# Optimization experiments

Hardware: AMD Instinct MI355X
Metric: run time of the kernel (lower is better)

The kernel has to match this reference:

```python
import jax, jax.numpy as jnp
import numpy as np

ALPHA = 1.0
BETA = 1.0
GAMMA = 1.0
EPS = 1e-08

D = 128      # feature / hash-code dim
N = 4096     # number of items


def setup_inputs() -> dict:
    key = jax.random.key(0)
    k = jax.random.split(key, 6)
    return {
        "SU": jax.random.uniform(k[0], (N, N, 1), dtype=jnp.float32),
        "SP": jax.random.uniform(k[1], (N, N, 1), dtype=jnp.float32),
        "SM": jax.random.uniform(k[2], (N, N, 1), dtype=jnp.float32),
        "FP": jax.random.uniform(k[3], (D, N), dtype=jnp.float32),
        "FM": jax.random.uniform(k[4], (D, N), dtype=jnp.float32),
        "B": jax.random.uniform(k[5], (D, N), dtype=jnp.float32),
    }


def reference(SU, SP, SM, FP, FM, B):
    # IRSC: Omega_U = FP^T FM / 2, sum over all (i,j) of -S*Omega + log(1+Omega)
    omega_u = jnp.einsum('di,dj->ij', FP, FM) * 0.5          # [N, N]
    loss_irsc = jnp.sum(-SU[:, :, 0] * omega_u + jnp.log1p(omega_u))

    # IASC: same form on FP^T FP and FM^T FM, with epsilon inside the log
    omega_p = jnp.einsum('di,dj->ij', FP, FP) * 0.5
    omega_m = jnp.einsum('di,dj->ij', FM, FM) * 0.5
    loss_sp = jnp.sum(-SP[:, :, 0] * omega_p + jnp.log(1.0 + omega_p + EPS))
    loss_sm = jnp.sum(-SM[:, :, 0] * omega_m + jnp.log(1.0 + omega_m + EPS))
    loss_iasc = loss_sp + loss_sm

    # BQC: Frobenius norms (not squared)
    loss_bqc = jnp.sqrt(jnp.sum((FP - B) ** 2)) + jnp.sqrt(jnp.sum((FM - B) ** 2))

    # FDC: ||F @ ones||_F^2 = sum over rows of (row-sum)^2
    loss_fdc = jnp.sum(jnp.sum(FP, axis=1) ** 2) + jnp.sum(jnp.sum(FM, axis=1) ** 2)

    return loss_irsc + ALPHA * loss_iasc + BETA * loss_bqc + GAMMA * loss_fdc
```

## Files before the change

kernel.cpp:

```cpp
#include <hip/hip_runtime.h>
#include <hip/hip_bf16.h>
#include <math.h>

#define NN 4096
#define DD 128

typedef __attribute__((ext_vector_type(8))) short bf16x8;
typedef __attribute__((ext_vector_type(4))) float f32x4;

__device__ __forceinline__ void gload_lds16(const float* g, float* l) {
    __builtin_amdgcn_global_load_lds((const __attribute__((address_space(1))) char*)g,
                                     (__attribute__((address_space(3))) char*)l, 16, 0, 0);
}

__global__ __launch_bounds__(256)
void convert_kernel(const float* __restrict__ FP, const float* __restrict__ FM,
                    __hip_bfloat16* __restrict__ FPb, __hip_bfloat16* __restrict__ FMb)
{
    const float* src = blockIdx.y ? FM : FP;
    __hip_bfloat16* dst = blockIdx.y ? FMb : FPb;
    const int t  = threadIdx.x;
    const int il = t & 127;
    const int dh = t >> 7;
    const int i  = blockIdx.x * 128 + il;
    #pragma unroll
    for (int it = 0; it < 8; ++it) {
        const int d0 = dh * 64 + it * 8;
        union { __hip_bfloat162 h[4]; bf16x8 v; } p;
        #pragma unroll
        for (int j = 0; j < 4; ++j) {
            const float a = src[(long)(d0 + 2*j)     * NN + i];
            const float b = src[(long)(d0 + 2*j + 1) * NN + i];
            p.h[j] = __float22bfloat162_rn(make_float2(a, b));
        }
        *(bf16x8*)&dst[(long)i * DD + d0] = p.v;
    }
}

__global__ __launch_bounds__(256, 2)
void gemm_loss_mfma2(const float* __restrict__ SU, const float* __restrict__ SP,
                     const float* __restrict__ SM,
                     const __hip_bfloat16* __restrict__ FPb,
                     const __hip_bfloat16* __restrict__ FMb,
                     double* __restrict__ accum)
{
    __shared__ float sS[4][64 * 64];
    __shared__ float red[4];
    const int t    = threadIdx.x;
    const int lane = t & 63, wid = t >> 6;
    const int wr   = wid >> 1, wc = wid & 1;
    const int l15  = lane & 15, l4 = lane >> 4;
    const int z    = blockIdx.z;
    const float* S  = (z == 0) ? SU : (z == 1) ? SP : SM;
    const short* Fa = (const short*)((z == 2) ? FMb : FPb);
    const short* Fb = (const short*)((z == 0) ? FMb : (z == 1) ? FPb : (const __hip_bfloat16*)FMb);
    const float eps = (z == 0) ? 0.0f : 1e-8f;
    const int i0 = blockIdx.y * 128;
    const int j0 = blockIdx.x * 128;

    bf16x8 af[4][4], bg[4][4];
    {
        const long ibase = (long)(i0 + wr * 64 + l15) * DD;
        const long jbase = (long)(j0 + wc * 64 + l15) * DD;
        #pragma unroll
        for (int kb = 0; kb < 4; ++kb) {
            const int ko = kb * 32 + l4 * 8;
            #pragma unroll
            for (int m = 0; m < 4; ++m) {
                af[kb][m] = *(const bf16x8*)&Fa[ibase + (long)m * 16 * DD + ko];
                bg[kb][m] = *(const bf16x8*)&Fb[jbase + (long)m * 16 * DD + ko];
            }
        }
    }

    {
        float* qb = sS[wid];
        const float* gb = S + (long)(i0 + wr * 64 + l4) * NN + j0 + wc * 64 + l15 * 4;
        #pragma unroll
        for (int q = 0; q < 16; ++q)
            gload_lds16(gb + (long)q * 4 * NN, qb + q * 256);
    }
    __builtin_amdgcn_sched_barrier(0);

    f32x4 acc[4][4] = {};
    #pragma unroll
    for (int kb = 0; kb < 4; ++kb)
        #pragma unroll
        for (int m = 0; m < 4; ++m)
            #pragma unroll
            for (int n = 0; n < 4; ++n)
                acc[m][n] = __builtin_amdgcn_mfma_f32_16x16x32_bf16(af[kb][m], bg[kb][n], acc[m][n], 0, 0, 0);

    asm volatile("s_waitcnt vmcnt(0)" ::: "memory");
    __builtin_amdgcn_sched_barrier(0);

    float lsum = 0.f;
    const float* q = sS[wid];
    #pragma unroll
    for (int m = 0; m < 4; ++m)
        #pragma unroll
        for (int n = 0; n < 4; ++n) {
            const int base = (m * 16 + l4 * 4) * 64 + n * 16 + l15;
            #pragma unroll
            for (int r = 0; r < 4; ++r) {
                const float s = q[base + r * 64];
                const float o = 0.5f * acc[m][n][r];
                lsum += fmaf(-s, o, __logf(1.0f + o + eps));
            }
        }

    float v = lsum;
    #pragma unroll
    for (int off = 32; off; off >>= 1) v += __shfl_down(v, off);
    if ((t & 63) == 0) red[t >> 6] = v;
    __syncthreads();
    if (t == 0) {
        const float tot = red[0] + red[1] + red[2] + red[3];
        atomicAdd(accum, (double)tot);
    }
}

__global__ __launch_bounds__(256, 2)
void gemm_loss_mfma(const float* __restrict__ S, const float* __restrict__ F1,
                    const float* __restrict__ F2, float eps, double* __restrict__ accum)
{
    __shared__ char lds[2][128 * 256];
    __shared__ float red[4];
    const int t  = threadIdx.x;
    const int i0 = blockIdx.y * 128;
    const int j0 = blockIdx.x * 128;
    {
        const int il   = t & 127;
        const int half = t >> 7;
        const float* c1 = F1 + i0 + il;
        const float* c2 = F2 + j0 + il;
        char* r1 = lds[0] + il * 256;
        char* r2 = lds[1] + il * 256;
        #pragma unroll
        for (int it = 0; it < 8; ++it) {
            const int q  = half * 8 + it;
            const int d0 = q * 8;
            float a[8], b[8];
            #pragma unroll
            for (int j = 0; j < 8; ++j) {
                a[j] = c1[(long)(d0 + j) * NN];
                b[j] = c2[(long)(d0 + j) * NN];
            }
            union { __hip_bfloat162 h[4]; bf16x8 v; } pa, pb;
            #pragma unroll
            for (int j = 0; j < 4; ++j) {
                pa.h[j] = __float22bfloat162_rn(make_float2(a[2*j], a[2*j+1]));
                pb.h[j] = __float22bfloat162_rn(make_float2(b[2*j], b[2*j+1]));
            }
            const int off = (q ^ (il & 15)) << 4;
            *(bf16x8*)(r1 + off) = pa.v;
            *(bf16x8*)(r2 + off) = pb.v;
        }
    }
    __syncthreads();
    const int lane = t & 63;
    const int wid  = t >> 6;
    const int wr   = wid >> 1, wc = wid & 1;
    const int l15  = lane & 15, l4 = lane >> 4;
    float sreg[4][4][4];
    #pragma unroll
    for (int am = 0; am < 4; ++am)
        #pragma unroll
        for (int r = 0; r < 4; ++r) {
            const long gi   = (long)(i0 + wr * 64 + am * 16 + l4 * 4 + r);
            const long base = gi * NN + j0 + wc * 64 + l15;
            #pragma unroll
            for (int bn = 0; bn < 4; ++bn)
                sreg[am][bn][r] = S[base + bn * 16];
        }
    f32x4 acc[4][4] = {};
    #pragma unroll
    for (int kb = 0; kb < 4; ++kb) {
        bf16x8 af[4], bgr[4];
        #pragma unroll
        for (int m = 0; m < 4; ++m) {
            const int ia = wr * 64 + m * 16 + l15;
            af[m] = *(const bf16x8*)(lds[0] + ia * 256 + (((kb * 4 + l4) ^ l15) << 4));
            const int jb = wc * 64 + m * 16 + l15;
            bgr[m] = *(const bf16x8*)(lds[1] + jb * 256 + (((kb * 4 + l4) ^ l15) << 4));
        }
        #pragma unroll
        for (int m = 0; m < 4; ++m)
            #pragma unroll
            for (int n = 0; n < 4; ++n)
                acc[m][n] = __builtin_amdgcn_mfma_f32_16x16x32_bf16(af[m], bgr[n], acc[m][n], 0, 0, 0);
    }
    float lsum = 0.f;
    #pragma unroll
    for (int m = 0; m < 4; ++m)
        #pragma unroll
        for (int n = 0; n < 4; ++n)
            #pragma unroll
            for (int r = 0; r < 4; ++r) {
                const float o = 0.5f * acc[m][n][r];
                lsum += fmaf(-sreg[m][n][r], o, __logf(1.0f + o + eps));
            }
    float v = lsum;
    #pragma unroll
    for (int off = 32; off; off >>= 1) v += __shfl_down(v, off);
    if ((t & 63) == 0) red[t >> 6] = v;
    __syncthreads();
    if (t == 0) {
        const float tot = red[0] + red[1] + red[2] + red[3];
        atomicAdd(accum, (double)tot);
    }
}

__global__ __launch_bounds__(256)
void bqc_kernel(const float* __restrict__ FP, const float* __restrict__ FM,
                const float* __restrict__ B, double* __restrict__ ws)
{
    __shared__ float red1[4], red2[4];
    const int n4 = DD * NN / 4;
    float s1 = 0.f, s2 = 0.f;
    for (int i = blockIdx.x * blockDim.x + threadIdx.x; i < n4;
         i += gridDim.x * blockDim.x) {
        const float4 p = ((const float4*)FP)[i];
        const float4 m = ((const float4*)FM)[i];
        const float4 b = ((const float4*)B)[i];
        float d;
        d = p.x - b.x; s1 += d * d;  d = p.y - b.y; s1 += d * d;
        d = p.z - b.z; s1 += d * d;  d = p.w - b.w; s1 += d * d;
        d = m.x - b.x; s2 += d * d;  d = m.y - b.y; s2 += d * d;
        d = m.z - b.z; s2 += d * d;  d = m.w - b.w; s2 += d * d;
    }
    const int t = threadIdx.x;
    #pragma unroll
    for (int off = 32; off; off >>= 1) {
        s1 += __shfl_down(s1, off);
        s2 += __shfl_down(s2, off);
    }
    if ((t & 63) == 0) { red1[t >> 6] = s1; red2[t >> 6] = s2; }
    __syncthreads();
    if (t == 0) {
        atomicAdd(&ws[1], (double)(red1[0] + red1[1] + red1[2] + red1[3]));
        atomicAdd(&ws[2], (double)(red2[0] + red2[1] + red2[2] + red2[3]));
    }
}

__global__ __launch_bounds__(256)
void fdc_kernel(const float* __restrict__ FP, const float* __restrict__ FM,
                double* __restrict__ ws)
{
    __shared__ float red[4];
    const float* F = (blockIdx.x >= DD) ? FM : FP;
    const int row = blockIdx.x & (DD - 1);
    float s = 0.f;
    const float4* rowp = (const float4*)&F[(long)row * NN];
    for (int i = threadIdx.x; i < NN / 4; i += blockDim.x) {
        const float4 v = rowp[i];
        s += v.x + v.y + v.z + v.w;
    }
    const int t = threadIdx.x;
    #pragma unroll
    for (int off = 32; off; off >>= 1) s += __shfl_down(s, off);
    if ((t & 63) == 0) red[t >> 6] = s;
    __syncthreads();
    if (t == 0) {
        const double rs = (double)(red[0] + red[1] + red[2] + red[3]);
        atomicAdd(&ws[3], rs * rs);
    }
}

__global__ void finalize_kernel(const double* __restrict__ ws, float* __restrict__ out)
{
    if (threadIdx.x == 0 && blockIdx.x == 0)
        out[0] = (float)(ws[0] + ws[3] + sqrt(ws[1]) + sqrt(ws[2]));
}

extern "C" void kernel_launch(void* const* d_in, const int* in_sizes, int n_in,
                              void* d_out, int out_size, void* d_ws, size_t ws_size,
                              hipStream_t stream)
{
    const float* SU = (const float*)d_in[0];
    const float* SP = (const float*)d_in[1];
    const float* SM = (const float*)d_in[2];
    const float* FP = (const float*)d_in[3];
    const float* FM = (const float*)d_in[4];
    const float* B  = (const float*)d_in[5];
    float*  out = (float*)d_out;
    double* ws  = (double*)d_ws;

    hipMemsetAsync(d_ws, 0, 4 * sizeof(double), stream);

    const size_t fb_bytes = (size_t)NN * DD * sizeof(__hip_bfloat16);
    const size_t need     = 4096 + 2 * fb_bytes;

    if (ws_size >= need) {
        __hip_bfloat16* FPb = (__hip_bfloat16*)((char*)d_ws + 4096);
        __hip_bfloat16* FMb = (__hip_bfloat16*)((char*)d_ws + 4096 + fb_bytes);
        convert_kernel<<<dim3(NN / 128, 2), 256, 0, stream>>>(FP, FM, FPb, FMb);
        gemm_loss_mfma2<<<dim3(NN / 128, NN / 128, 3), 256, 0, stream>>>(
            SU, SP, SM, FPb, FMb, ws);
    } else {
        dim3 grid(NN / 128, NN / 128);
        gemm_loss_mfma<<<grid, 256, 0, stream>>>(SU, FP, FM, 0.0f, ws);
        gemm_loss_mfma<<<grid, 256, 0, stream>>>(SP, FP, FP, 1e-8f, ws);
        gemm_loss_mfma<<<grid, 256, 0, stream>>>(SM, FM, FM, 1e-8f, ws);
    }
    bqc_kernel<<<512, 256, 0, stream>>>(FP, FM, B, ws);
    fdc_kernel<<<256, 256, 0, stream>>>(FP, FM, ws);
    finalize_kernel<<<1, 64, 0, stream>>>(ws, out);
}
```

Measured before the change: 98.69 us.

## Split loss into symmetric log-term GEMM and reassociated S·F dot-product pass

Splits the fused GEMM+loss into two kernels. The log1p term is computed over upper-triangular tiles only for the symmetric FP^T FP and FM^T FM cases, with off-diagonal tiles weighted by two. The -S*Omega term is reassociated as sum(F_a ⊙ (S · F_b^T)) and computed by a skinny MFMA kernel that streams S once, converted to bf16 on the fly. Atomics are spread over 16 padded slots to cut contention. This removes about a third of the log GEMM work, but S is now rounded to bf16, which adds precision error, and an extra conversion kernel is added.

```diff
diff --git a/kernel.cpp b/kernel.cpp
--- a/kernel.cpp
+++ b/kernel.cpp
@@ -8,17 +8,13 @@
 typedef __attribute__((ext_vector_type(8))) short bf16x8;
 typedef __attribute__((ext_vector_type(4))) float f32x4;
 
-__device__ __forceinline__ void gload_lds16(const float* g, float* l) {
-    __builtin_amdgcn_global_load_lds((const __attribute__((address_space(1))) char*)g,
-                                     (__attribute__((address_space(3))) char*)l, 16, 0, 0);
-}
 
 __global__ __launch_bounds__(256)
-void convert_kernel(const float* __restrict__ FP, const float* __restrict__ FM,
-                    __hip_bfloat16* __restrict__ FPb, __hip_bfloat16* __restrict__ FMb)
+void convert_t_kernel(const float* __restrict__ FP, const float* __restrict__ FM,
+                      __hip_bfloat16* __restrict__ FPt, __hip_bfloat16* __restrict__ FMt)
 {
     const float* src = blockIdx.y ? FM : FP;
-    __hip_bfloat16* dst = blockIdx.y ? FMb : FPb;
+    __hip_bfloat16* dst = blockIdx.y ? FMt : FPt;
     const int t  = threadIdx.x;
     const int il = t & 127;
     const int dh = t >> 7;
@@ -37,87 +33,197 @@
     }
 }
 
-__global__ __launch_bounds__(256, 2)
-void gemm_loss_mfma2(const float* __restrict__ SU, const float* __restrict__ SP,
-                     const float* __restrict__ SM,
-                     const __hip_bfloat16* __restrict__ FPb,
-                     const __hip_bfloat16* __restrict__ FMb,
-                     double* __restrict__ accum)
-{
-    __shared__ float sS[4][64 * 64];
-    __shared__ float red[4];
-    const int t    = threadIdx.x;
+__global__ __launch_bounds__(256)
+void convert_d_kernel(const float* __restrict__ FP, const float* __restrict__ FM,
+                      __hip_bfloat16* __restrict__ FPd, __hip_bfloat16* __restrict__ FMd)
+{
+    const int total = DD * NN / 4;
+    for (int idx = blockIdx.x * blockDim.x + threadIdx.x; idx < 2 * total;
+         idx += gridDim.x * blockDim.x) {
+        const bool second = idx >= total;
+        const float4 v = ((const float4*)(second ? FM : FP))[second ? idx - total : idx];
+        union { __hip_bfloat162 h[2]; uint2 u; } p;
+        p.h[0] = __float22bfloat162_rn(make_float2(v.x, v.y));
+        p.h[1] = __float22bfloat162_rn(make_float2(v.z, v.w));
+        ((uint2*)(second ? FMd : FPd))[second ? idx - total : idx] = p.u;
+    }
+}
+
+__global__ __launch_bounds__(256, 3)
+void log_kernel(const __hip_bfloat16* __restrict__ FPt_,
+                const __hip_bfloat16* __restrict__ FMt_, double* __restrict__ accum)
+{
+    const int bid = blockIdx.x;
+    int z, ti, tj;
+    if (bid < 1024) { z = 0; ti = bid >> 5; tj = bid & 31; }
+    else {
+        int q = bid - 1024;
+        z = 1 + (q >= 528);
+        int u = (q >= 528) ? q - 528 : q;
+        ti = 0;
+        while (u >= 32 - ti) { u -= 32 - ti; ++ti; }
+        tj = ti + u;
+    }
+    const short* Fa = (const short*)((z == 2) ? FMt_ : FPt_);
+    const short* Fb = (const short*)((z == 0) ? FMt_ : (z == 1) ? FPt_ : FMt_);
+    const float onep = 1.0f + ((z == 0) ? 0.0f : 1e-8f);
+
+    const int t = threadIdx.x;
     const int lane = t & 63, wid = t >> 6;
-    const int wr   = wid >> 1, wc = wid & 1;
-    const int l15  = lane & 15, l4 = lane >> 4;
-    const int z    = blockIdx.z;
+    const int wr = wid >> 1, wc = wid & 1;
+    const int l15 = lane & 15, l4 = lane >> 4;
+    const int i0 = ti * 128 + wr * 64;
+    const int j0 = tj * 128 + wc * 64;
+
+    const bool diagTile = (z > 0) && (ti == tj);
+    const bool skip     = diagTile && (wr > wc);
+    const bool perElem  = diagTile && (wr == wc);
+    const bool dbl      = (z > 0) && ((ti < tj) || (diagTile && wr < wc));
+
+    const short* pa = Fa + (long)(i0 + l15) * DD + l4 * 8;
+    const short* pb = Fb + (long)(j0 + l15) * DD + l4 * 8;
+
+    float lsum = 0.f;
+    if (!skip) {
+        bf16x8 Aa[4], Ab[4], Ba[4], Bb[4];
+        #pragma unroll
+        for (int m = 0; m < 4; ++m) {
+            Aa[m] = *(const bf16x8*)(pa + m * (16 * DD));
+            Ab[m] = *(const bf16x8*)(pb + m * (16 * DD));
+        }
+        f32x4 acc[4][4] = {};
+        #pragma unroll
+        for (int kb = 0; kb < 4; ++kb) {
+            if (kb == 0 || kb == 2) {
+                if (kb < 3) {
+                    #pragma unroll
+                    for (int m = 0; m < 4; ++m) {
+                        Ba[m] = *(const bf16x8*)(pa + m * (16 * DD) + (kb + 1) * 32);
+                        Bb[m] = *(const bf16x8*)(pb + m * (16 * DD) + (kb + 1) * 32);
+                    }
+                }
+                #pragma unroll
+                for (int m = 0; m < 4; ++m)
+                    #pragma unroll
+                    for (int n = 0; n < 4; ++n)
+                        acc[m][n] = __builtin_amdgcn_mfma_f32_16x16x32_bf16(Aa[m], Ab[n], acc[m][n], 0, 0, 0);
+            } else {
+                if (kb < 3) {
+                    #pragma unroll
+                    for (int m = 0; m < 4; ++m) {
+                        Aa[m] = *(const bf16x8*)(pa + m * (16 * DD) + (kb + 1) * 32);
+                        Ab[m] = *(const bf16x8*)(pb + m * (16 * DD) + (kb + 1) * 32);
+                    }
+                }
+                #pragma unroll
+                for (int m = 0; m < 4; ++m)
+                    #pragma unroll
+                    for (int n = 0; n < 4; ++n)
+                        acc[m][n] = __builtin_amdgcn_mfma_f32_16x16x32_bf16(Ba[m], Bb[n], acc[m][n], 0, 0, 0);
+            }
+        }
+        #pragma unroll
+        for (int m = 0; m < 4; ++m)
+            #pragma unroll
+            for (int n = 0; n < 4; ++n)
+                #pragma unroll
+                for (int r = 0; r < 4; ++r) {
+                    const float term = __logf(fmaf(0.5f, acc[m][n][r], onep));
+                    if (perElem) {
+                        const int il = m * 16 + l4 * 4 + r;
+                        const int jl = n * 16 + l15;
+                        const float w = (jl > il) ? 2.f : ((jl == il) ? 1.f : 0.f);
+                        lsum = fmaf(w, term, lsum);
+                    } else {
+                        lsum += term;
+                    }
+                }
+        if (dbl) lsum *= 2.f;
+    }
+
+    float v = lsum;
+    #pragma unroll
+    for (int off = 32; off; off >>= 1) v += __shfl_down(v, off);
+    if (lane == 0 && !skip)
+        atomicAdd(accum + ((bid & 15) << 3), (double)v);
+}
+
+__global__ __launch_bounds__(256, 3)
+void dot_kernel(const float* __restrict__ SU, const float* __restrict__ SP,
+                const float* __restrict__ SM,
+                const __hip_bfloat16* __restrict__ FPd_,
+                const __hip_bfloat16* __restrict__ FMd_,
+                const float* __restrict__ FPf, const float* __restrict__ FMf,
+                double* __restrict__ accum)
+{
+    const int t = threadIdx.x;
+    const int lane = t & 63, wid = t >> 6;
+    const int l15 = lane & 15, l4 = lane >> 4;
+    const int w = blockIdx.x * 4 + wid;
+    const int z = w >> 10;
+    const int rem = w & 1023;
+    const int ks = rem & 7;
+    const int is = rem >> 3;
+
     const float* S  = (z == 0) ? SU : (z == 1) ? SP : SM;
-    const short* Fa = (const short*)((z == 2) ? FMb : FPb);
-    const short* Fb = (const short*)((z == 0) ? FMb : (z == 1) ? FPb : (const __hip_bfloat16*)FMb);
-    const float eps = (z == 0) ? 0.0f : 1e-8f;
-    const int i0 = blockIdx.y * 128;
-    const int j0 = blockIdx.x * 128;
-
-    bf16x8 af[4][4], bg[4][4];
-    {
-        const long ibase = (long)(i0 + wr * 64 + l15) * DD;
-        const long jbase = (long)(j0 + wc * 64 + l15) * DD;
-        #pragma unroll
-        for (int kb = 0; kb < 4; ++kb) {
-            const int ko = kb * 32 + l4 * 8;
-            #pragma unroll
-            for (int m = 0; m < 4; ++m) {
-                af[kb][m] = *(const bf16x8*)&Fa[ibase + (long)m * 16 * DD + ko];
-                bg[kb][m] = *(const bf16x8*)&Fb[jbase + (long)m * 16 * DD + ko];
-            }
-        }
-    }
-
-    {
-        float* qb = sS[wid];
-        const float* gb = S + (long)(i0 + wr * 64 + l4) * NN + j0 + wc * 64 + l15 * 4;
-        #pragma unroll
-        for (int q = 0; q < 16; ++q)
-            gload_lds16(gb + (long)q * 4 * NN, qb + q * 256);
-    }
-    __builtin_amdgcn_sched_barrier(0);
-
-    f32x4 acc[4][4] = {};
-    #pragma unroll
-    for (int kb = 0; kb < 4; ++kb)
-        #pragma unroll
-        for (int m = 0; m < 4; ++m)
-            #pragma unroll
-            for (int n = 0; n < 4; ++n)
-                acc[m][n] = __builtin_amdgcn_mfma_f32_16x16x32_bf16(af[kb][m], bg[kb][n], acc[m][n], 0, 0, 0);
-
-    asm volatile("s_waitcnt vmcnt(0)" ::: "memory");
-    __builtin_amdgcn_sched_barrier(0);
+    const short* Fb = (const short*)((z == 1) ? FPd_ : FMd_);
+    const float* Fa = (z == 2) ? FMf : FPf;
+
+    const int i0 = is * 32;
+    const int jb = ks * 512;
+
+    f32x4 acc[2][8] = {};
+    const float* srow0 = S + (long)(i0 + l15) * NN + l4 * 8;
+    const float* srow1 = srow0 + 16 * NN;
+    const short* fbp   = Fb + (long)l15 * NN + l4 * 8;
+
+    #pragma unroll 2
+    for (int c = 0; c < 16; ++c) {
+        const int jc = jb + c * 32;
+        bf16x8 aS[2];
+        {
+            const float4 lo0 = *(const float4*)(srow0 + jc);
+            const float4 hi0 = *(const float4*)(srow0 + jc + 4);
+            const float4 lo1 = *(const float4*)(srow1 + jc);
+            const float4 hi1 = *(const float4*)(srow1 + jc + 4);
+            union { __hip_bfloat162 h[4]; bf16x8 v; } p0, p1;
+            p0.h[0] = __float22bfloat162_rn(make_float2(lo0.x, lo0.y));
+            p0.h[1] = __float22bfloat162_rn(make_float2(lo0.z, lo0.w));
+            p0.h[2] = __float22bfloat162_rn(make_float2(hi0.x, hi0.y));
+            p0.h[3] = __float22bfloat162_rn(make_float2(hi0.z, hi0.w));
+            p1.h[0] = __float22bfloat162_rn(make_float2(lo1.x, lo1.y));
+            p1.h[1] = __float22bfloat162_rn(make_float2(lo1.z, lo1.w));
+            p1.h[2] = __float22bfloat162_rn(make_float2(hi1.x, hi1.y));
+            p1.h[3] = __float22bfloat162_rn(make_float2(hi1.z, hi1.w));
+            aS[0] = p0.v; aS[1] = p1.v;
+        }
+        bf16x8 bF[8];
+        #pragma unroll
+        for (int n = 0; n < 8; ++n)
+            bF[n] = *(const bf16x8*)(fbp + (long)n * 16 * NN + jc);
+        #pragma unroll
+        for (int m = 0; m < 2; ++m)
+            #pragma unroll
+            for (int n = 0; n < 8; ++n)
+                acc[m][n] = __builtin_amdgcn_mfma_f32_16x16x32_bf16(aS[m], bF[n], acc[m][n], 0, 0, 0);
+    }
 
     float lsum = 0.f;
-    const float* q = sS[wid];
-    #pragma unroll
-    for (int m = 0; m < 4; ++m)
-        #pragma unroll
-        for (int n = 0; n < 4; ++n) {
-            const int base = (m * 16 + l4 * 4) * 64 + n * 16 + l15;
-            #pragma unroll
-            for (int r = 0; r < 4; ++r) {
-                const float s = q[base + r * 64];
-                const float o = 0.5f * acc[m][n][r];
-                lsum += fmaf(-s, o, __logf(1.0f + o + eps));
-            }
+    #pragma unroll
+    for (int m = 0; m < 2; ++m)
+        #pragma unroll
+        for (int n = 0; n < 8; ++n) {
+            const long drow = (long)(n * 16 + l15) * NN + i0 + m * 16 + l4 * 4;
+            #pragma unroll
+            for (int r = 0; r < 4; ++r)
+                lsum = fmaf(acc[m][n][r], Fa[drow + r], lsum);
         }
 
     float v = lsum;
     #pragma unroll
     for (int off = 32; off; off >>= 1) v += __shfl_down(v, off);
-    if ((t & 63) == 0) red[t >> 6] = v;
-    __syncthreads();
-    if (t == 0) {
-        const float tot = red[0] + red[1] + red[2] + red[3];
-        atomicAdd(accum, (double)tot);
-    }
+    if (lane == 0)
+        atomicAdd(accum + ((blockIdx.x & 15) << 3), (double)(-0.5 * v));
 }
 
 __global__ __launch_bounds__(256, 2)
@@ -167,11 +273,11 @@
     for (int am = 0; am < 4; ++am)
         #pragma unroll
         for (int r = 0; r < 4; ++r) {
-            const long gi   = (long)(i0 + wr * 64 + am * 16 + l4 * 4 + r);
-            const long base = gi * NN + j0 + wc * 64 + l15;
+            const long gi    = (long)(i0 + wr * 64 + am * 16 + l4 * 4 + r);
+            const long basep = gi * NN + j0 + wc * 64 + l15;
             #pragma unroll
             for (int bn = 0; bn < 4; ++bn)
-                sreg[am][bn][r] = S[base + bn * 16];
+                sreg[am][bn][r] = S[basep + bn * 16];
         }
     f32x4 acc[4][4] = {};
     #pragma unroll
@@ -181,8 +287,8 @@
         for (int m = 0; m < 4; ++m) {
             const int ia = wr * 64 + m * 16 + l15;
             af[m] = *(const bf16x8*)(lds[0] + ia * 256 + (((kb * 4 + l4) ^ l15) << 4));
-            const int jb = wc * 64 + m * 16 + l15;
-            bgr[m] = *(const bf16x8*)(lds[1] + jb * 256 + (((kb * 4 + l4) ^ l15) << 4));
+            const int jbq = wc * 64 + m * 16 + l15;
+            bgr[m] = *(const bf16x8*)(lds[1] + jbq * 256 + (((kb * 4 + l4) ^ l15) << 4));
         }
         #pragma unroll
         for (int m = 0; m < 4; ++m)
@@ -238,8 +344,8 @@
     if ((t & 63) == 0) { red1[t >> 6] = s1; red2[t >> 6] = s2; }
     __syncthreads();
     if (t == 0) {
-        atomicAdd(&ws[1], (double)(red1[0] + red1[1] + red1[2] + red1[3]));
-        atomicAdd(&ws[2], (double)(red2[0] + red2[1] + red2[2] + red2[3]));
+        atomicAdd(&ws[128], (double)(red1[0] + red1[1] + red1[2] + red1[3]));
+        atomicAdd(&ws[129], (double)(red2[0] + red2[1] + red2[2] + red2[3]));
     }
 }
 
@@ -263,14 +369,18 @@
     __syncthreads();
     if (t == 0) {
         const double rs = (double)(red[0] + red[1] + red[2] + red[3]);
-        atomicAdd(&ws[3], rs * rs);
+        atomicAdd(&ws[130], rs * rs);
     }
 }
 
 __global__ void finalize_kernel(const double* __restrict__ ws, float* __restrict__ out)
 {
-    if (threadIdx.x == 0 && blockIdx.x == 0)
-        out[0] = (float)(ws[0] + ws[3] + sqrt(ws[1]) + sqrt(ws[2]));
+    if (threadIdx.x == 0 && blockIdx.x == 0) {
+        double s = 0.0;
+        #pragma unroll
+        for (int k = 0; k < 16; ++k) s += ws[k * 8];
+        out[0] = (float)(s + ws[130] + sqrt(ws[128]) + sqrt(ws[129]));
+    }
 }
 
 extern "C" void kernel_launch(void* const* d_in, const int* in_sizes, int n_in,
@@ -286,17 +396,21 @@
     float*  out = (float*)d_out;
     double* ws  = (double*)d_ws;
 
-    hipMemsetAsync(d_ws, 0, 4 * sizeof(double), stream);
-
-    const size_t fb_bytes = (size_t)NN * DD * sizeof(__hip_bfloat16);
-    const size_t need     = 4096 + 2 * fb_bytes;
+    hipMemsetAsync(d_ws, 0, 4096, stream);
+
+    const size_t fb = (size_t)NN * DD * sizeof(__hip_bfloat16);
+    const size_t need = 4096 + 4 * fb;
 
     if (ws_size >= need) {
-        __hip_bfloat16* FPb = (__hip_bfloat16*)((char*)d_ws + 4096);
-        __hip_bfloat16* FMb = (__hip_bfloat16*)((char*)d_ws + 4096 + fb_bytes);
-        convert_kernel<<<dim3(NN / 128, 2), 256, 0, stream>>>(FP, FM, FPb, FMb);
-        gemm_loss_mfma2<<<dim3(NN / 128, NN / 128, 3), 256, 0, stream>>>(
-            SU, SP, SM, FPb, FMb, ws);
+        char* base = (char*)d_ws + 4096;
+        __hip_bfloat16* FPt = (__hip_bfloat16*)(base);
+        __hip_bfloat16* FMt = (__hip_bfloat16*)(base + fb);
+        __hip_bfloat16* FPd = (__hip_bfloat16*)(base + 2 * fb);
+        __hip_bfloat16* FMd = (__hip_bfloat16*)(base + 3 * fb);
+        convert_t_kernel<<<dim3(NN / 128, 2), 256, 0, stream>>>(FP, FM, FPt, FMt);
+        convert_d_kernel<<<512, 256, 0, stream>>>(FP, FM, FPd, FMd);
+        log_kernel<<<2080, 256, 0, stream>>>(FPt, FMt, ws);
+        dot_kernel<<<768, 256, 0, stream>>>(SU, SP, SM, FPd, FMd, FP, FM, ws);
     } else {
         dim3 grid(NN / 128, NN / 128);
         gemm_loss_mfma<<<grid, 256, 0, stream>>>(SU, FP, FM, 0.0f, ws);
```

New measurement: 149.3 us. 1.51x slower.

## Make fused GEMM-loss kernel persistent with per-wave double-buffered S prefetch

Applied to the files above, without the earlier changes.

Replaces the 3D grid of 128x128 tiles with a persistent 512-block grid. Each wave walks 12 tiles of 64x32 covering all three similarity matrices. While it computes the current tile, the wave prefetches the next tile's S block into a second LDS buffer with global_load_lds, waiting with a partial vmcnt. Per-block LDS reduction and syncthreads are removed, and per-wave double atomics are spread across 16 padded slots to reduce contention, with finalize summing them. The trade-off is smaller tiles: bf16 F fragments are reloaded from global/L2 far more often, and MFMA reuse per load drops.

```diff
diff --git a/kernel.cpp b/kernel.cpp
--- a/kernel.cpp
+++ b/kernel.cpp
@@ -8,17 +8,18 @@
 typedef __attribute__((ext_vector_type(8))) short bf16x8;
 typedef __attribute__((ext_vector_type(4))) float f32x4;
 
+
 __device__ __forceinline__ void gload_lds16(const float* g, float* l) {
     __builtin_amdgcn_global_load_lds((const __attribute__((address_space(1))) char*)g,
                                      (__attribute__((address_space(3))) char*)l, 16, 0, 0);
 }
 
 __global__ __launch_bounds__(256)
-void convert_kernel(const float* __restrict__ FP, const float* __restrict__ FM,
-                    __hip_bfloat16* __restrict__ FPb, __hip_bfloat16* __restrict__ FMb)
+void convert_t_kernel(const float* __restrict__ FP, const float* __restrict__ FM,
+                      __hip_bfloat16* __restrict__ FPt, __hip_bfloat16* __restrict__ FMt)
 {
     const float* src = blockIdx.y ? FM : FP;
-    __hip_bfloat16* dst = blockIdx.y ? FMb : FPb;
+    __hip_bfloat16* dst = blockIdx.y ? FMt : FPt;
     const int t  = threadIdx.x;
     const int il = t & 127;
     const int dh = t >> 7;
@@ -38,86 +39,91 @@
 }
 
 __global__ __launch_bounds__(256, 2)
-void gemm_loss_mfma2(const float* __restrict__ SU, const float* __restrict__ SP,
+void gemm_loss_fused(const float* __restrict__ SU, const float* __restrict__ SP,
                      const float* __restrict__ SM,
-                     const __hip_bfloat16* __restrict__ FPb,
-                     const __hip_bfloat16* __restrict__ FMb,
+                     const __hip_bfloat16* __restrict__ FPt_,
+                     const __hip_bfloat16* __restrict__ FMt_,
                      double* __restrict__ accum)
 {
-    __shared__ float sS[4][64 * 64];
-    __shared__ float red[4];
-    const int t    = threadIdx.x;
-    const int lane = t & 63, wid = t >> 6;
-    const int wr   = wid >> 1, wc = wid & 1;
+    __shared__ float sS[4][2][64 * 32];
+    const int t0   = threadIdx.x;
+    const int lane = t0 & 63, wid = t0 >> 6;
     const int l15  = lane & 15, l4 = lane >> 4;
-    const int z    = blockIdx.z;
-    const float* S  = (z == 0) ? SU : (z == 1) ? SP : SM;
-    const short* Fa = (const short*)((z == 2) ? FMb : FPb);
-    const short* Fb = (const short*)((z == 0) ? FMb : (z == 1) ? FPb : (const __hip_bfloat16*)FMb);
-    const float eps = (z == 0) ? 0.0f : 1e-8f;
-    const int i0 = blockIdx.y * 128;
-    const int j0 = blockIdx.x * 128;
-
-    bf16x8 af[4][4], bg[4][4];
-    {
-        const long ibase = (long)(i0 + wr * 64 + l15) * DD;
-        const long jbase = (long)(j0 + wc * 64 + l15) * DD;
+    const int w    = blockIdx.x * 4 + wid;
+    const short* FPt = (const short*)FPt_;
+    const short* FMt = (const short*)FMt_;
+
+#define STAGE(G_, buf_)                                                        \
+    {                                                                          \
+        const int z_  = (G_) >> 13;                                            \
+        const float* S_ = (z_ == 0) ? SU : (z_ == 1) ? SP : SM;                \
+        const int i0_ = (((G_) >> 7) & 63) << 6;                               \
+        const int j0_ = ((G_) & 127) << 5;                                     \
+        const float* src_ = S_ + (long)(i0_ + (lane >> 3)) * NN + j0_ + (lane & 7) * 4; \
+        _Pragma("unroll")                                                      \
+        for (int q_ = 0; q_ < 8; ++q_)                                         \
+            gload_lds16(src_ + (long)q_ * 8 * NN, &sS[wid][buf_][q_ * 256]);   \
+    }
+
+    float lsum = 0.f;
+    STAGE(w, 0);
+
+    #pragma unroll 1
+    for (int t = 0; t < 12; ++t) {
+        const int G  = w + t * 2048;
+        const int z  = G >> 13;
+        const int i0 = ((G >> 7) & 63) << 6;
+        const int j0 = (G & 127) << 5;
+        const short* Fa = (z == 2) ? FMt : FPt;
+        const short* Fb = (z == 1) ? FPt : FMt;
+        const float onep = (z == 0) ? 1.0f : 1.0f + 1e-8f;
+
+        bf16x8 af[4][4], bg[4][2];
         #pragma unroll
         for (int kb = 0; kb < 4; ++kb) {
-            const int ko = kb * 32 + l4 * 8;
-            #pragma unroll
-            for (int m = 0; m < 4; ++m) {
-                af[kb][m] = *(const bf16x8*)&Fa[ibase + (long)m * 16 * DD + ko];
-                bg[kb][m] = *(const bf16x8*)&Fb[jbase + (long)m * 16 * DD + ko];
-            }
-        }
-    }
-
-    {
-        float* qb = sS[wid];
-        const float* gb = S + (long)(i0 + wr * 64 + l4) * NN + j0 + wc * 64 + l15 * 4;
-        #pragma unroll
-        for (int q = 0; q < 16; ++q)
-            gload_lds16(gb + (long)q * 4 * NN, qb + q * 256);
-    }
-    __builtin_amdgcn_sched_barrier(0);
-
-    f32x4 acc[4][4] = {};
-    #pragma unroll
-    for (int kb = 0; kb < 4; ++kb)
+            #pragma unroll
+            for (int m = 0; m < 4; ++m)
+                af[kb][m] = *(const bf16x8*)&Fa[(long)(i0 + m * 16 + l15) * DD + kb * 32 + l4 * 8];
+            #pragma unroll
+            for (int n = 0; n < 2; ++n)
+                bg[kb][n] = *(const bf16x8*)&Fb[(long)(j0 + n * 16 + l15) * DD + kb * 32 + l4 * 8];
+        }
+
+        if (t < 11) STAGE(G + 2048, (t + 1) & 1);
+
+        __builtin_amdgcn_sched_barrier(0);
+        if (t < 11) asm volatile("s_waitcnt vmcnt(8)");
+        else        asm volatile("s_waitcnt vmcnt(0)");
+        __builtin_amdgcn_sched_barrier(0);
+
+        f32x4 acc[4][2] = {};
+        #pragma unroll
+        for (int kb = 0; kb < 4; ++kb)
+            #pragma unroll
+            for (int m = 0; m < 4; ++m)
+                #pragma unroll
+                for (int n = 0; n < 2; ++n)
+                    acc[m][n] = __builtin_amdgcn_mfma_f32_16x16x32_bf16(af[kb][m], bg[kb][n], acc[m][n], 0, 0, 0);
+
+        const float* curS = &sS[wid][t & 1][0];
         #pragma unroll
         for (int m = 0; m < 4; ++m)
             #pragma unroll
-            for (int n = 0; n < 4; ++n)
-                acc[m][n] = __builtin_amdgcn_mfma_f32_16x16x32_bf16(af[kb][m], bg[kb][n], acc[m][n], 0, 0, 0);
-
-    asm volatile("s_waitcnt vmcnt(0)" ::: "memory");
-    __builtin_amdgcn_sched_barrier(0);
-
-    float lsum = 0.f;
-    const float* q = sS[wid];
-    #pragma unroll
-    for (int m = 0; m < 4; ++m)
-        #pragma unroll
-        for (int n = 0; n < 4; ++n) {
-            const int base = (m * 16 + l4 * 4) * 64 + n * 16 + l15;
-            #pragma unroll
-            for (int r = 0; r < 4; ++r) {
-                const float s = q[base + r * 64];
-                const float o = 0.5f * acc[m][n][r];
-                lsum += fmaf(-s, o, __logf(1.0f + o + eps));
-            }
-        }
+            for (int n = 0; n < 2; ++n)
+                #pragma unroll
+                for (int r = 0; r < 4; ++r) {
+                    const float s = curS[(m * 16 + l4 * 4 + r) * 32 + n * 16 + l15];
+                    const float o = 0.5f * acc[m][n][r];
+                    lsum += fmaf(-s, o, __logf(o + onep));
+                }
+    }
+#undef STAGE
 
     float v = lsum;
     #pragma unroll
     for (int off = 32; off; off >>= 1) v += __shfl_down(v, off);
-    if ((t & 63) == 0) red[t >> 6] = v;
-    __syncthreads();
-    if (t == 0) {
-        const float tot = red[0] + red[1] + red[2] + red[3];
-        atomicAdd(accum, (double)tot);
-    }
+    if (lane == 0)
+        atomicAdd(accum + ((w & 15) << 3), (double)v);
 }
 
 __global__ __launch_bounds__(256, 2)
@@ -167,11 +173,11 @@
     for (int am = 0; am < 4; ++am)
         #pragma unroll
         for (int r = 0; r < 4; ++r) {
-            const long gi   = (long)(i0 + wr * 64 + am * 16 + l4 * 4 + r);
-            const long base = gi * NN + j0 + wc * 64 + l15;
+            const long gi    = (long)(i0 + wr * 64 + am * 16 + l4 * 4 + r);
+            const long basep = gi * NN + j0 + wc * 64 + l15;
             #pragma unroll
             for (int bn = 0; bn < 4; ++bn)
-                sreg[am][bn][r] = S[base + bn * 16];
+                sreg[am][bn][r] = S[basep + bn * 16];
         }
     f32x4 acc[4][4] = {};
     #pragma unroll
@@ -181,8 +187,8 @@
         for (int m = 0; m < 4; ++m) {
             const int ia = wr * 64 + m * 16 + l15;
             af[m] = *(const bf16x8*)(lds[0] + ia * 256 + (((kb * 4 + l4) ^ l15) << 4));
-            const int jb = wc * 64 + m * 16 + l15;
-            bgr[m] = *(const bf16x8*)(lds[1] + jb * 256 + (((kb * 4 + l4) ^ l15) << 4));
+            const int jbq = wc * 64 + m * 16 + l15;
+            bgr[m] = *(const bf16x8*)(lds[1] + jbq * 256 + (((kb * 4 + l4) ^ l15) << 4));
         }
         #pragma unroll
         for (int m = 0; m < 4; ++m)
@@ -238,8 +244,8 @@
     if ((t & 63) == 0) { red1[t >> 6] = s1; red2[t >> 6] = s2; }
     __syncthreads();
     if (t == 0) {
-        atomicAdd(&ws[1], (double)(red1[0] + red1[1] + red1[2] + red1[3]));
-        atomicAdd(&ws[2], (double)(red2[0] + red2[1] + red2[2] + red2[3]));
+        atomicAdd(&ws[128], (double)(red1[0] + red1[1] + red1[2] + red1[3]));
+        atomicAdd(&ws[129], (double)(red2[0] + red2[1] + red2[2] + red2[3]));
     }
 }
 
@@ -263,14 +269,18 @@
     __syncthreads();
     if (t == 0) {
         const double rs = (double)(red[0] + red[1] + red[2] + red[3]);
-        atomicAdd(&ws[3], rs * rs);
+        atomicAdd(&ws[130], rs * rs);
     }
 }
 
 __global__ void finalize_kernel(const double* __restrict__ ws, float* __restrict__ out)
 {
-    if (threadIdx.x == 0 && blockIdx.x == 0)
-        out[0] = (float)(ws[0] + ws[3] + sqrt(ws[1]) + sqrt(ws[2]));
+    if (threadIdx.x == 0 && blockIdx.x == 0) {
+        double s = 0.0;
+        #pragma unroll
+        for (int k = 0; k < 16; ++k) s += ws[k * 8];
+        out[0] = (float)(s + ws[130] + sqrt(ws[128]) + sqrt(ws[129]));
+    }
 }
 
 extern "C" void kernel_launch(void* const* d_in, const int* in_sizes, int n_in,
@@ -286,17 +296,17 @@
     float*  out = (float*)d_out;
     double* ws  = (double*)d_ws;
 
-    hipMemsetAsync(d_ws, 0, 4 * sizeof(double), stream);
-
-    const size_t fb_bytes = (size_t)NN * DD * sizeof(__hip_bfloat16);
-    const size_t need     = 4096 + 2 * fb_bytes;
+    hipMemsetAsync(d_ws, 0, 4096, stream);
+
+    const size_t fb   = (size_t)NN * DD * sizeof(__hip_bfloat16);
+    const size_t need = 4096 + 2 * fb;
 
     if (ws_size >= need) {
-        __hip_bfloat16* FPb = (__hip_bfloat16*)((char*)d_ws + 4096);
-        __hip_bfloat16* FMb = (__hip_bfloat16*)((char*)d_ws + 4096 + fb_bytes);
-        convert_kernel<<<dim3(NN / 128, 2), 256, 0, stream>>>(FP, FM, FPb, FMb);
-        gemm_loss_mfma2<<<dim3(NN / 128, NN / 128, 3), 256, 0, stream>>>(
-            SU, SP, SM, FPb, FMb, ws);
+        char* base = (char*)d_ws + 4096;
+        __hip_bfloat16* FPt = (__hip_bfloat16*)(base);
+        __hip_bfloat16* FMt = (__hip_bfloat16*)(base + fb);
+        convert_t_kernel<<<dim3(NN / 128, 2), 256, 0, stream>>>(FP, FM, FPt, FMt);
+        gemm_loss_fused<<<512, 256, 0, stream>>>(SU, SP, SM, FPt, FMt, ws);
     } else {
         dim3 grid(NN / 128, NN / 128);
         gemm_loss_mfma<<<grid, 256, 0, stream>>>(SU, FP, FM, 0.0f, ws);
```

Result: slower. 123.5 us (+25.1%).
